# Kernel tuning notes

Hardware: AMD Instinct MI355X
Metric: run time of the kernel (lower is better)

The kernel has to match this reference:

```python
import jax, jax.numpy as jnp
import numpy as np

N_DRUG, N_DIS, E, D = 10000, 15000, 1048576, 128

def setup_inputs() -> dict:
    key = jax.random.key(0)
    k = jax.random.split(key, 6)
    return {
        "z_drug": jax.random.normal(k[0], (N_DRUG, D), dtype=jnp.float32),
        "z_disease": jax.random.normal(k[1], (N_DIS, D), dtype=jnp.float32),
        "row": jax.random.randint(k[2], (E,), 0, N_DRUG),
        "col": jax.random.randint(k[3], (E,), 0, N_DIS),
        "W1": jax.random.normal(k[4], (2 * D, D), dtype=jnp.float32) * (1.0 / np.sqrt(2 * D)),
        "b1": jnp.zeros((D,), dtype=jnp.float32),
        "W2": jax.random.normal(k[5], (D, 1), dtype=jnp.float32) * (1.0 / np.sqrt(D)),
        "b2": jnp.zeros((1,), dtype=jnp.float32),
    }

def reference(z_drug, z_disease, row, col, W1, b1, W2, b2):
    # gather per-edge embeddings and concatenate: [E, 2D]
    z = jnp.concatenate([z_drug[row], z_disease[col]], axis=-1)
    h = jax.nn.relu(z @ W1 + b1)          # [E, D]
    out = h @ W2 + b2                      # [E, 1]
    return out.reshape(-1)                 # [E]
```

## Files before the change

kernel.cpp:

```cpp
#include <hip/hip_runtime.h>

typedef __attribute__((ext_vector_type(8))) short short8;
typedef __attribute__((ext_vector_type(4))) float floatx4;
typedef _Float16 half8 __attribute__((ext_vector_type(8)));
typedef _Float16 half4 __attribute__((ext_vector_type(4)));

static __device__ __forceinline__ unsigned short f2bf(float x) {
    unsigned int u = __builtin_bit_cast(unsigned int, x);
    unsigned int r = (u + 0x7FFFu + ((u >> 16) & 1u)) >> 16;
    return (unsigned short)r;
}

__global__ void prep_w1(const float* __restrict__ W1, unsigned short* __restrict__ w1t) {
    int i = blockIdx.x * 256 + threadIdx.x;
    int n = i >> 8;
    int k = i & 255;
    w1t[n * 256 + k] = f2bf(W1[k * 128 + n]);
}

__global__ __launch_bounds__(256, 2) void factor_gemm(
    const float* __restrict__ zd, const float* __restrict__ zs,
    const unsigned short* __restrict__ w1t, const float* __restrict__ b1,
    _Float16* __restrict__ ud, _Float16* __restrict__ us,
    int ndrows, int nsrows, int ntd)
{
    const int tid  = threadIdx.x;
    const int lane = tid & 63;
    const int wave = tid >> 6;
    const int wh   = wave >> 1;
    const int we   = wave & 1;
    const int l15  = lane & 15;
    const int quad = lane >> 4;

    const int b = blockIdx.x;
    const bool isD = (b < ntd);
    const float* __restrict__ z = isD ? zd : zs;
    _Float16* __restrict__ u = isD ? ud : us;
    const int nrows = isD ? ndrows : nsrows;
    const int m0    = (isD ? b : b - ntd) * 64;
    const int koff0 = isD ? 0 : 128;

    short8 wfrag[16];
    #pragma unroll
    for (int s = 0; s < 4; ++s)
        #pragma unroll
        for (int mt = 0; mt < 4; ++mt)
            wfrag[s * 4 + mt] = *reinterpret_cast<const short8*>(
                &w1t[(size_t)(wh * 64 + mt * 16 + l15) * 256 + koff0 + s * 32 + quad * 8]);

    floatx4 acc[2][4];
    #pragma unroll
    for (int mt = 0; mt < 4; ++mt) {
        floatx4 bb = *reinterpret_cast<const floatx4*>(&b1[wh * 64 + mt * 16 + quad * 4]);
        bb *= 0.5f;
        acc[0][mt] = bb;
        acc[1][mt] = bb;
    }

    int rowi[2], rowc[2];
    #pragma unroll
    for (int et = 0; et < 2; ++et) {
        rowi[et] = m0 + we * 32 + et * 16 + l15;
        rowc[et] = rowi[et] < nrows ? rowi[et] : nrows - 1;
    }

    #pragma unroll
    for (int s = 0; s < 4; ++s) {
        short8 bf[2];
        #pragma unroll
        for (int et = 0; et < 2; ++et) {
            const float* src = &z[(size_t)rowc[et] * 128 + s * 32 + quad * 8];
            floatx4 lo = *reinterpret_cast<const floatx4*>(src);
            floatx4 hi = *reinterpret_cast<const floatx4*>(src + 4);
            short8 t;
            t[0] = (short)f2bf(lo[0]); t[1] = (short)f2bf(lo[1]);
            t[2] = (short)f2bf(lo[2]); t[3] = (short)f2bf(lo[3]);
            t[4] = (short)f2bf(hi[0]); t[5] = (short)f2bf(hi[1]);
            t[6] = (short)f2bf(hi[2]); t[7] = (short)f2bf(hi[3]);
            bf[et] = t;
        }
        #pragma unroll
        for (int et = 0; et < 2; ++et)
            #pragma unroll
            for (int mt = 0; mt < 4; ++mt)
                acc[et][mt] = __builtin_amdgcn_mfma_f32_16x16x32_bf16(
                    wfrag[s * 4 + mt], bf[et], acc[et][mt], 0, 0, 0);
    }

    #pragma unroll
    for (int et = 0; et < 2; ++et) {
        if (rowi[et] < nrows) {
            #pragma unroll
            for (int mt = 0; mt < 4; ++mt) {
                half4 hv;
                #pragma unroll
                for (int rr = 0; rr < 4; ++rr) hv[rr] = (_Float16)acc[et][mt][rr];
                *reinterpret_cast<half4*>(
                    &u[(size_t)rowi[et] * 128 + wh * 64 + mt * 16 + quad * 4]) = hv;
            }
        }
    }
}

__global__ __launch_bounds__(256, 4) void edge_eval(
    const _Float16* __restrict__ ud, const _Float16* __restrict__ us,
    const int* __restrict__ row, const int* __restrict__ col,
    const float* __restrict__ w2, const float* __restrict__ b2,
    float* __restrict__ out, int nchunks)
{
    const int tid  = threadIdx.x;
    const int lane = tid & 63;
    const int wave = tid >> 6;
    const int le   = lane >> 2;
    const int q    = lane & 3;

    float w2r[32];
    #pragma unroll
    for (int i = 0; i < 8; ++i)
        *reinterpret_cast<floatx4*>(&w2r[i * 4]) =
            *reinterpret_cast<const floatx4*>(&w2[q * 32 + i * 4]);
    const float b2v = b2[0];

    const int G = gridDim.x;
    long t = blockIdx.x;
    if (t >= nchunks) return;
    long eg = t * 64 + wave * 16 + le;
    int r = row[eg], c = col[eg];

    while (t < nchunks) {
        const _Float16* up = ud + (size_t)r * 128 + q * 32;
        const _Float16* vp = us + (size_t)c * 128 + q * 32;
        half8 uu[4], vv[4];
        #pragma unroll
        for (int i = 0; i < 4; ++i) {
            uu[i] = *reinterpret_cast<const half8*>(up + i * 8);
            vv[i] = *reinterpret_cast<const half8*>(vp + i * 8);
        }

        long tn = t + G;
        int rn = 0, cn = 0;
        if (tn < nchunks) {
            long egn = tn * 64 + wave * 16 + le;
            rn = row[egn];
            cn = col[egn];
        }

        float acc = 0.f;
        #pragma unroll
        for (int i = 0; i < 4; ++i) {
            half8 s8 = uu[i] + vv[i];
            s8 = __builtin_elementwise_max(s8, (half8)(_Float16)0.f);
            #pragma unroll
            for (int j = 0; j < 8; ++j)
                acc += (float)s8[j] * w2r[i * 8 + j];
        }

        acc += __shfl_xor(acc, 1);
        acc += __shfl_xor(acc, 2);
        if (q == 0) out[eg] = acc + b2v;

        t = tn;
        eg = tn * 64 + wave * 16 + le;
        r = rn; c = cn;
    }
}

extern "C" void kernel_launch(void* const* d_in, const int* in_sizes, int n_in,
                              void* d_out, int out_size, void* d_ws, size_t ws_size,
                              hipStream_t stream) {
    const float* zd = (const float*)d_in[0];
    const float* zs = (const float*)d_in[1];
    const int*   row = (const int*)d_in[2];
    const int*   col = (const int*)d_in[3];
    const float* W1 = (const float*)d_in[4];
    const float* b1 = (const float*)d_in[5];
    const float* w2 = (const float*)d_in[6];
    const float* b2 = (const float*)d_in[7];
    float* out = (float*)d_out;

    const int nd = in_sizes[0];
    const int ns = in_sizes[1];
    const int E  = in_sizes[2];
    const int ndrows = nd / 128;
    const int nsrows = ns / 128;

    unsigned short* w1t = (unsigned short*)d_ws;
    _Float16* ud = (_Float16*)((char*)d_ws + 128 * 256 * sizeof(unsigned short));
    _Float16* us = ud + (size_t)ndrows * 128;

    hipLaunchKernelGGL(prep_w1, dim3(128), dim3(256), 0, stream, W1, w1t);

    const int ntd = (ndrows + 63) / 64;
    const int nts = (nsrows + 63) / 64;
    hipLaunchKernelGGL(factor_gemm, dim3(ntd + nts), dim3(256), 0, stream,
                       zd, zs, w1t, b1, ud, us, ndrows, nsrows, ntd);

    const int nchunks = E / 64;
    const int egrid = nchunks < 2048 ? nchunks : 2048;
    hipLaunchKernelGGL(edge_eval, dim3(egrid), dim3(256), 0, stream,
                       ud, us, row, col, w2, b2, out, nchunks);
}
```

Before: 142.7 us.

## Double-buffer edge gathers and spread each edge across eight lanes

The edge kernel now gives each edge 8 lanes instead of 4, so each lane loads two strided 16-byte fp16 chunks per table and the partial sums are reduced with an extra shuffle. The loop is software-pipelined with two register buffers, so the gather for the next chunk is issued before the current one is computed, and indices are prefetched two chunks ahead. The intent is more memory-level parallelism for the random gathers, at the cost of more registers and an extra shuffle. Chunks shrink to 32 edges and the grid is fixed at 2048 blocks with no clamp, which assumes nchunks is at least 2048.

```diff
diff --git a/kernel.cpp b/kernel.cpp
--- a/kernel.cpp
+++ b/kernel.cpp
@@ -111,58 +111,86 @@
     const int tid  = threadIdx.x;
     const int lane = tid & 63;
     const int wave = tid >> 6;
-    const int le   = lane >> 2;
-    const int q    = lane & 3;
-
-    float w2r[32];
-    #pragma unroll
-    for (int i = 0; i < 8; ++i)
-        *reinterpret_cast<floatx4*>(&w2r[i * 4]) =
-            *reinterpret_cast<const floatx4*>(&w2[q * 32 + i * 4]);
+    const int le   = lane >> 3;
+    const int q    = lane & 7;
+    const int lslot = wave * 8 + le;
+
+    float w2r[16];
+    #pragma unroll
+    for (int i = 0; i < 2; ++i) {
+        *reinterpret_cast<floatx4*>(&w2r[i * 8]) =
+            *reinterpret_cast<const floatx4*>(&w2[i * 64 + q * 8]);
+        *reinterpret_cast<floatx4*>(&w2r[i * 8 + 4]) =
+            *reinterpret_cast<const floatx4*>(&w2[i * 64 + q * 8 + 4]);
+    }
     const float b2v = b2[0];
-
     const int G = gridDim.x;
-    long t = blockIdx.x;
+
+    int t = blockIdx.x;
     if (t >= nchunks) return;
-    long eg = t * 64 + wave * 16 + le;
-    int r = row[eg], c = col[eg];
-
-    while (t < nchunks) {
-        const _Float16* up = ud + (size_t)r * 128 + q * 32;
-        const _Float16* vp = us + (size_t)c * 128 + q * 32;
-        half8 uu[4], vv[4];
-        #pragma unroll
-        for (int i = 0; i < 4; ++i) {
-            uu[i] = *reinterpret_cast<const half8*>(up + i * 8);
-            vv[i] = *reinterpret_cast<const half8*>(vp + i * 8);
+
+#define GATHER(U, V, rr, cc)                                                      \
+    {                                                                             \
+        _Pragma("unroll")                                                         \
+        for (int i = 0; i < 2; ++i) {                                             \
+            U[i] = *reinterpret_cast<const half8*>(&ud[(rr) * 128 + i * 64 + q * 8]); \
+            V[i] = *reinterpret_cast<const half8*>(&us[(cc) * 128 + i * 64 + q * 8]); \
+        }                                                                         \
+    }
+
+#define COMPUTE(U, V, tt)                                                         \
+    {                                                                             \
+        float acc = 0.f;                                                          \
+        _Pragma("unroll")                                                         \
+        for (int i = 0; i < 2; ++i) {                                             \
+            half8 s8 = U[i] + V[i];                                               \
+            s8 = __builtin_elementwise_max(s8, (half8)(_Float16)0.f);             \
+            _Pragma("unroll")                                                     \
+            for (int j = 0; j < 8; ++j)                                           \
+                acc += (float)s8[j] * w2r[i * 8 + j];                             \
+        }                                                                         \
+        acc += __shfl_xor(acc, 1);                                                \
+        acc += __shfl_xor(acc, 2);                                                \
+        acc += __shfl_xor(acc, 4);                                                \
+        if (q == 0) out[(tt) * 32 + lslot] = acc + b2v;                           \
+    }
+
+    int rA = row[t * 32 + lslot], cA = col[t * 32 + lslot];
+    half8 uA[2], vA[2], uB[2], vB[2];
+    GATHER(uA, vA, rA, cA)
+    int rB = 0, cB = 0;
+    {
+        int t1 = t + G;
+        if (t1 < nchunks) { rB = row[t1 * 32 + lslot]; cB = col[t1 * 32 + lslot]; }
+    }
+
+    while (true) {
+        const int tB = t + G, tA2 = t + 2 * G;
+
+        if (tB < nchunks) GATHER(uB, vB, rB, cB)
+
+        int rA2 = 0, cA2 = 0;
+        if (tA2 < nchunks) { rA2 = row[tA2 * 32 + lslot]; cA2 = col[tA2 * 32 + lslot]; }
+
+        COMPUTE(uA, vA, t)
+
+        if (tB >= nchunks) break;
+
+        if (tA2 < nchunks) GATHER(uA, vA, rA2, cA2)
+
+        {
+            int t3 = t + 3 * G;
+            rB = 0; cB = 0;
+            if (t3 < nchunks) { rB = row[t3 * 32 + lslot]; cB = col[t3 * 32 + lslot]; }
         }
 
-        long tn = t + G;
-        int rn = 0, cn = 0;
-        if (tn < nchunks) {
-            long egn = tn * 64 + wave * 16 + le;
-            rn = row[egn];
-            cn = col[egn];
-        }
-
-        float acc = 0.f;
-        #pragma unroll
-        for (int i = 0; i < 4; ++i) {
-            half8 s8 = uu[i] + vv[i];
-            s8 = __builtin_elementwise_max(s8, (half8)(_Float16)0.f);
-            #pragma unroll
-            for (int j = 0; j < 8; ++j)
-                acc += (float)s8[j] * w2r[i * 8 + j];
-        }
-
-        acc += __shfl_xor(acc, 1);
-        acc += __shfl_xor(acc, 2);
-        if (q == 0) out[eg] = acc + b2v;
-
-        t = tn;
-        eg = tn * 64 + wave * 16 + le;
-        r = rn; c = cn;
-    }
+        COMPUTE(uB, vB, tB)
+
+        if (tA2 >= nchunks) break;
+        t = tA2;
+    }
+#undef GATHER
+#undef COMPUTE
 }
 
 extern "C" void kernel_launch(void* const* d_in, const int* in_sizes, int n_in,
@@ -195,8 +223,8 @@
     hipLaunchKernelGGL(factor_gemm, dim3(ntd + nts), dim3(256), 0, stream,
                        zd, zs, w1t, b1, ud, us, ndrows, nsrows, ntd);
 
-    const int nchunks = E / 64;
-    const int egrid = nchunks < 2048 ? nchunks : 2048;
+    const int nchunks = E / 32;
+    const int egrid = 2048;
     hipLaunchKernelGGL(edge_eval, dim3(egrid), dim3(256), 0, stream,
                        ud, us, row, col, w2, b2, out, nchunks);
 }
```

After: 126.4 us. 11.4% less time.

## Software-pipeline edge gathers with 4-slot ring and fdot2 reduction

Applied to the files above, without the earlier changes.

Rewrites the edge evaluation loop so that each block processes a fixed count of 32-edge chunks through a 4-slot register ring. Index loads run two chunks ahead and row gathers run three chunks ahead of compute, which keeps several gathers in flight per wave. Each edge is now handled by 8 lanes instead of 4, each loading 16-byte pieces at offsets 0 and 64, and the dot product with W2 uses packed half fdot2. The grid is fixed at 1024 blocks and NC = nchunks/G assumes an even split, so any leftover chunks would be dropped when E is not a multiple of 32*1024.

```diff
diff --git a/kernel.cpp b/kernel.cpp
--- a/kernel.cpp
+++ b/kernel.cpp
@@ -4,6 +4,7 @@
 typedef __attribute__((ext_vector_type(4))) float floatx4;
 typedef _Float16 half8 __attribute__((ext_vector_type(8)));
 typedef _Float16 half4 __attribute__((ext_vector_type(4)));
+typedef _Float16 half2v __attribute__((ext_vector_type(2)));
 
 static __device__ __forceinline__ unsigned short f2bf(float x) {
     unsigned int u = __builtin_bit_cast(unsigned int, x);
@@ -111,58 +112,103 @@
     const int tid  = threadIdx.x;
     const int lane = tid & 63;
     const int wave = tid >> 6;
-    const int le   = lane >> 2;
-    const int q    = lane & 3;
-
-    float w2r[32];
-    #pragma unroll
-    for (int i = 0; i < 8; ++i)
-        *reinterpret_cast<floatx4*>(&w2r[i * 4]) =
-            *reinterpret_cast<const floatx4*>(&w2[q * 32 + i * 4]);
+    const int le   = lane >> 3;
+    const int q    = lane & 7;
+    const int lslot = wave * 8 + le;
+
+#if __has_builtin(__builtin_amdgcn_fdot2)
+    half2v w2h[8];
+    #pragma unroll
+    for (int i = 0; i < 2; ++i)
+        #pragma unroll
+        for (int p = 0; p < 4; ++p) {
+            half2v t;
+            t[0] = (_Float16)w2[i * 64 + q * 8 + 2 * p];
+            t[1] = (_Float16)w2[i * 64 + q * 8 + 2 * p + 1];
+            w2h[i * 4 + p] = t;
+        }
+#else
+    float w2r[16];
+    #pragma unroll
+    for (int i = 0; i < 2; ++i) {
+        *reinterpret_cast<floatx4*>(&w2r[i * 8]) =
+            *reinterpret_cast<const floatx4*>(&w2[i * 64 + q * 8]);
+        *reinterpret_cast<floatx4*>(&w2r[i * 8 + 4]) =
+            *reinterpret_cast<const floatx4*>(&w2[i * 64 + q * 8 + 4]);
+    }
+#endif
     const float b2v = b2[0];
-
     const int G = gridDim.x;
-    long t = blockIdx.x;
-    if (t >= nchunks) return;
-    long eg = t * 64 + wave * 16 + le;
-    int r = row[eg], c = col[eg];
-
-    while (t < nchunks) {
-        const _Float16* up = ud + (size_t)r * 128 + q * 32;
-        const _Float16* vp = us + (size_t)c * 128 + q * 32;
-        half8 uu[4], vv[4];
-        #pragma unroll
-        for (int i = 0; i < 4; ++i) {
-            uu[i] = *reinterpret_cast<const half8*>(up + i * 8);
-            vv[i] = *reinterpret_cast<const half8*>(vp + i * 8);
-        }
-
-        long tn = t + G;
-        int rn = 0, cn = 0;
-        if (tn < nchunks) {
-            long egn = tn * 64 + wave * 16 + le;
-            rn = row[egn];
-            cn = col[egn];
-        }
-
-        float acc = 0.f;
-        #pragma unroll
-        for (int i = 0; i < 4; ++i) {
-            half8 s8 = uu[i] + vv[i];
-            s8 = __builtin_elementwise_max(s8, (half8)(_Float16)0.f);
-            #pragma unroll
-            for (int j = 0; j < 8; ++j)
-                acc += (float)s8[j] * w2r[i * 8 + j];
-        }
-
-        acc += __shfl_xor(acc, 1);
-        acc += __shfl_xor(acc, 2);
-        if (q == 0) out[eg] = acc + b2v;
-
-        t = tn;
-        eg = tn * 64 + wave * 16 + le;
-        r = rn; c = cn;
-    }
+    const int b = blockIdx.x;
+    const int NC = nchunks / G;
+
+    int ridx[4], cidx[4];
+    half8 Ur[4][2], Vr[4][2];
+
+#define LIDX(slot, j)                                                          \
+    if ((j) < NC) {                                                            \
+        int e = (b + (j) * G) * 32 + lslot;                                    \
+        ridx[slot] = row[e]; cidx[slot] = col[e];                              \
+    }
+
+#define GATH(slot, j)                                                          \
+    if ((j) < NC) {                                                            \
+        const _Float16* up = ud + (size_t)ridx[slot] * 128 + q * 8;            \
+        const _Float16* vp = us + (size_t)cidx[slot] * 128 + q * 8;            \
+        Ur[slot][0] = *reinterpret_cast<const half8*>(up);                     \
+        Ur[slot][1] = *reinterpret_cast<const half8*>(up + 64);                \
+        Vr[slot][0] = *reinterpret_cast<const half8*>(vp);                     \
+        Vr[slot][1] = *reinterpret_cast<const half8*>(vp + 64);                \
+    }
+
+#if __has_builtin(__builtin_amdgcn_fdot2)
+#define DOT(slot, accv)                                                        \
+    _Pragma("unroll")                                                          \
+    for (int i = 0; i < 2; ++i) {                                              \
+        half8 s8 = Ur[slot][i] + Vr[slot][i];                                  \
+        s8 = __builtin_elementwise_max(s8, (half8)(_Float16)0.f);              \
+        _Pragma("unroll")                                                      \
+        for (int p = 0; p < 4; ++p) {                                          \
+            half2v pr; pr[0] = s8[2 * p]; pr[1] = s8[2 * p + 1];               \
+            accv = __builtin_amdgcn_fdot2(pr, w2h[i * 4 + p], accv, false);    \
+        }                                                                      \
+    }
+#else
+#define DOT(slot, accv)                                                        \
+    _Pragma("unroll")                                                          \
+    for (int i = 0; i < 2; ++i) {                                              \
+        half8 s8 = Ur[slot][i] + Vr[slot][i];                                  \
+        s8 = __builtin_elementwise_max(s8, (half8)(_Float16)0.f);              \
+        _Pragma("unroll")                                                      \
+        for (int j2 = 0; j2 < 8; ++j2)                                         \
+            accv += (float)s8[j2] * w2r[i * 8 + j2];                           \
+    }
+#endif
+
+#define COMP(slot, j)                                                          \
+    if ((j) < NC) {                                                            \
+        float acc = 0.f;                                                       \
+        DOT(slot, acc)                                                         \
+        acc += __shfl_xor(acc, 1);                                             \
+        acc += __shfl_xor(acc, 2);                                             \
+        acc += __shfl_xor(acc, 4);                                             \
+        if (q == 0) out[(b + (j) * G) * 32 + lslot] = acc + b2v;               \
+    }
+
+    LIDX(0, 0) LIDX(1, 1) LIDX(2, 2)
+    GATH(0, 0) GATH(1, 1) GATH(2, 2)
+    LIDX(3, 3) LIDX(0, 4)
+
+    for (int jb = 0; jb < NC; jb += 4) {
+        GATH(3, jb + 3) LIDX(1, jb + 5) COMP(0, jb)
+        GATH(0, jb + 4) LIDX(2, jb + 6) COMP(1, jb + 1)
+        GATH(1, jb + 5) LIDX(3, jb + 7) COMP(2, jb + 2)
+        GATH(2, jb + 6) LIDX(0, jb + 8) COMP(3, jb + 3)
+    }
+#undef LIDX
+#undef GATH
+#undef DOT
+#undef COMP
 }
 
 extern "C" void kernel_launch(void* const* d_in, const int* in_sizes, int n_in,
@@ -195,8 +241,8 @@
     hipLaunchKernelGGL(factor_gemm, dim3(ntd + nts), dim3(256), 0, stream,
                        zd, zs, w1t, b1, ud, us, ndrows, nsrows, ntd);
 
-    const int nchunks = E / 64;
-    const int egrid = nchunks < 2048 ? nchunks : 2048;
+    const int nchunks = E / 32;
+    const int egrid = 1024;
     hipLaunchKernelGGL(edge_eval, dim3(egrid), dim3(256), 0, stream,
                        ud, us, row, col, w2, b2, out, nchunks);
 }
```

Result: faster. 126.3 us (-11.5%).
